# Performance work log

Measured on AMD Instinct MI355X. Metric: run time of the kernel, lower is better.

Reference implementation:

```python
import jax, jax.numpy as jnp
import numpy as np

G, NPG, K = 128, 1024, 16          # graphs, nodes per graph, kNN neighbors
NB_IN = 3
SLOPE = 0.01                        # torch.nn.LeakyReLU default negative_slope


def leaky(v):
    return jnp.where(v >= 0, v, SLOPE * v)


def knn_idx(pos, k):
    """pos: [G, n, 3] -> neighbor indices [G, n, k] within each graph, self excluded.
    Matches torch_geometric.nn.knn_graph (k nearest by Euclidean distance)."""
    sq = jnp.sum(pos * pos, axis=-1)                              # [G, n]
    d2 = sq[:, :, None] + sq[:, None, :] - 2.0 * jnp.einsum('gnd,gmd->gnm', pos, pos)
    n = pos.shape[1]
    d2 = d2 + jnp.eye(n, dtype=pos.dtype) * 1e9                   # exclude self-loops
    _, idx = jax.lax.top_k(-d2, k)                                # k smallest distances
    return idx


def edge_conv(h, idx, W1, b1, W2, b2):
    """EdgeConv with aggr='add': sum_j mlp(cat([x_i, x_j - x_i])).
    h: [G, n, F], idx: [G, n, k] -> [G, n, out]"""
    xj = jax.vmap(lambda hg, ig: hg[ig])(h, idx)                  # gather: [G, n, k, F]
    xi = jnp.broadcast_to(h[:, :, None, :], xj.shape)
    m = jnp.concatenate([xi, xj - xi], axis=-1)                   # [G, n, k, 2F]
    m = leaky(m @ W1 + b1)
    m = leaky(m @ W2 + b2)
    return jnp.sum(m, axis=2)                                     # scatter-add over k


def _linear_init(key, fin, fout):
    kw, kb = jax.random.split(key)
    lim = 1.0 / np.sqrt(fin)
    W = jax.random.uniform(kw, (fin, fout), jnp.float32, -lim, lim)
    b = jax.random.uniform(kb, (fout,), jnp.float32, -lim, lim)
    return W, b


def setup_inputs() -> dict:
    key = jax.random.key(0)
    ks = jax.random.split(key, 10)
    x = jax.random.normal(ks[0], (G * NPG, NB_IN), jnp.float32)
    batch = jnp.repeat(jnp.arange(G, dtype=jnp.int32), NPG)
    # layer 1 MLP: [2*3 -> 16 -> 16]; layer 2 MLP: [2*16 -> 16 -> 16]
    W1a, b1a = _linear_init(ks[1], 2 * NB_IN, 16)
    W2a, b2a = _linear_init(ks[2], 16, 16)
    W1b, b1b = _linear_init(ks[3], 2 * 16, 16)
    W2b, b2b = _linear_init(ks[4], 16, 16)
    # post-processing: [3+16+16=35 -> 16 -> 16]
    Wp1, bp1 = _linear_init(ks[5], 35, 16)
    Wp2, bp2 = _linear_init(ks[6], 16, 16)
    # readout: [16*3 poolings = 48 -> 128 -> 10]
    Wr1, br1 = _linear_init(ks[7], 48, 128)
    Wr2, br2 = _linear_init(ks[8], 128, 10)
    return {"x": x, "batch": batch,
            "W1a": W1a, "b1a": b1a, "W2a": W2a, "b2a": b2a,
            "W1b": W1b, "b1b": b1b, "W2b": W2b, "b2b": b2b,
            "Wp1": Wp1, "bp1": bp1, "Wp2": Wp2, "bp2": bp2,
            "Wr1": Wr1, "br1": br1, "Wr2": Wr2, "br2": br2}


def reference(x, batch, W1a, b1a, W2a, b2a, W1b, b1b, W2b, b2b,
              Wp1, bp1, Wp2, bp2, Wr1, br1, Wr2, br2):
    # equal-sized graphs sorted by batch id -> reshape to [G, n, F]
    h = x.reshape(G, NPG, -1)
    skips = [h]
    for (W1, b1, W2, b2) in ((W1a, b1a, W2a, b2a), (W1b, b1b, W2b, b2b)):
        idx = knn_idx(h[..., :3], K)       # features_subset = slice(0, 3)
        h = edge_conv(h, idx, W1, b1, W2, b2)
        skips.append(h)
    h = jnp.concatenate(skips, axis=-1)    # [G, n, 35]
    h = leaky(h @ Wp1 + bp1)
    h = leaky(h @ Wp2 + bp2)               # [G, n, 16]
    pooled = jnp.concatenate([h.min(axis=1), h.max(axis=1), h.mean(axis=1)], axis=-1)  # [G, 48]
    out = leaky(pooled @ Wr1 + br1) @ Wr2 + br2                   # [G, 10]
    return out
```

## Files before the change

### kernel.cpp

```cpp
#include <hip/hip_runtime.h>

#define NG 128
#define NN 1024
#define KK 16
#define HALF 512
#define PCAP 8
#define PMAX 16
#define SLOPE 0.01f
#define FINF 3.0e38f

typedef unsigned short u16;

__device__ __forceinline__ float leaky(float v) {
    return v >= 0.0f ? v : SLOPE * v;
}

__device__ __forceinline__ void sorted_insert(float (&bd)[KK], int (&bi)[KK],
                                              float d, int j) {
    bool c[KK];
#pragma unroll
    for (int t = 0; t < KK; ++t) c[t] = d < bd[t];
#pragma unroll
    for (int t = KK - 1; t >= 1; --t) {
        bd[t] = c[t] ? (c[t - 1] ? bd[t - 1] : d) : bd[t];
        bi[t] = c[t] ? (c[t - 1] ? bi[t - 1] : j) : bi[t];
    }
    bd[0] = c[0] ? d : bd[0];
    bi[0] = c[0] ? j : bi[0];
}

__device__ __forceinline__ void knn_scan_half(const float4* __restrict__ posq,
                                              float* __restrict__ pend_d,
                                              u16* __restrict__ pend_j,
                                              int tid, int i, int jlo,
                                              float (&bd)[KK], int (&bi)[KK]) {
    const float4 meq = posq[i];
    const float mex = -2.0f * meq.x, mey = -2.0f * meq.y, mez = -2.0f * meq.z;
    const float mew = meq.w;
#pragma unroll
    for (int t = 0; t < KK; ++t) { bd[t] = FINF; bi[t] = 0; }
    float T = FINF;
    int cnt = 0;

    for (int j0 = jlo; j0 < jlo + HALF; j0 += 8) {
        float4 p[8];
#pragma unroll
        for (int u = 0; u < 8; ++u) p[u] = posq[j0 + u];
#pragma unroll
        for (int u = 0; u < 8; ++u) {
            const int j = j0 + u;
            float d2 = fmaf(mex, p[u].x, fmaf(mey, p[u].y,
                          fmaf(mez, p[u].z, mew + p[u].w)));
            bool pass = (d2 < T) && (j != i);
            if (pass) {
                pend_d[tid + 256 * cnt] = d2;
                pend_j[tid + 256 * cnt] = (u16)j;
                ++cnt;
            }
        }
        if (__any(cnt >= PCAP)) {
#pragma unroll 1
            for (int s = 0; s < PMAX - 1; ++s) {
                float d = (s < cnt) ? pend_d[tid + 256 * s] : FINF;
                int j = pend_j[tid + 256 * s];
                if (__any(d < bd[KK - 1])) sorted_insert(bd, bi, d, j);
            }
            cnt = 0;
            T = bd[KK - 1];
        }
    }
#pragma unroll 1
    for (int s = 0; s < PCAP; ++s) {
        float d = (s < cnt) ? pend_d[tid + 256 * s] : FINF;
        int j = pend_j[tid + 256 * s];
        if (__any(d < bd[KK - 1])) sorted_insert(bd, bi, d, j);
    }
}

__device__ __forceinline__ void knn_body(const float4* __restrict__ posq,
                                         float* __restrict__ buf_d,
                                         u16* __restrict__ buf_j,
                                         int g, int chunk, int tid,
                                         u16* __restrict__ idx) {
    const int q = tid & 127;
    const int half = tid >> 7;
    const int i = chunk * 128 + q;

    float bd[KK];
    int bi[KK];
    knn_scan_half(posq, buf_d, buf_j, tid, i, half * HALF, bd, bi);

#pragma unroll
    for (int t = 0; t < KK; ++t) {
        buf_d[tid + 256 * t] = bd[t];
        buf_j[tid + 256 * t] = (u16)bi[t];
    }
    __syncthreads();

    if (tid < 128) {
        int ia = 0, ib = 0;
        unsigned int pack[8];
#pragma unroll
        for (int k = 0; k < KK; ++k) {
            float da = buf_d[tid + 256 * ia];
            float db = buf_d[(tid + 128) + 256 * ib];
            bool ta = da <= db;
            unsigned int j = ta ? (unsigned int)buf_j[tid + 256 * ia]
                               : (unsigned int)buf_j[(tid + 128) + 256 * ib];
            ia += ta ? 1 : 0;
            ib += ta ? 0 : 1;
            if ((k & 1) == 0) pack[k >> 1] = j;
            else pack[k >> 1] |= j << 16;
        }
        uint4* o4 = (uint4*)(idx + ((size_t)g * NN + i) * KK);
        o4[0] = make_uint4(pack[0], pack[1], pack[2], pack[3]);
        o4[1] = make_uint4(pack[4], pack[5], pack[6], pack[7]);
    }
}

__global__ __launch_bounds__(256) void knn1(
    const float* __restrict__ x, u16* __restrict__ idx)
{
    __shared__ float4 posq[NN];
    __shared__ float buf_d[256 * PMAX];
    __shared__ u16 buf_j[256 * PMAX];

    const int g = blockIdx.x >> 3;
    const int chunk = blockIdx.x & 7;
    const int tid = threadIdx.x;

    for (int n = tid; n < NN; n += 256) {
        const float* xp = x + (size_t)(g * NN + n) * 3;
        float px = xp[0], py = xp[1], pz = xp[2];
        posq[n] = make_float4(px, py, pz, px * px + py * py + pz * pz);
    }
    __syncthreads();

    knn_body(posq, buf_d, buf_j, g, chunk, tid, idx);
}

__global__ __launch_bounds__(256) void knn2(
    const float* __restrict__ h1, u16* __restrict__ idx)
{
    __shared__ float4 posq[NN];
    __shared__ float buf_d[256 * PMAX];
    __shared__ u16 buf_j[256 * PMAX];

    const int g = blockIdx.x >> 3;
    const int chunk = blockIdx.x & 7;
    const int tid = threadIdx.x;

    for (int n = tid; n < NN; n += 256) {
        const float4 a = *(const float4*)(h1 + (size_t)(g * NN + n) * 16);
        posq[n] = make_float4(a.x, a.y, a.z, a.x * a.x + a.y * a.y + a.z * a.z);
    }
    __syncthreads();

    knn_body(posq, buf_d, buf_j, g, chunk, tid, idx);
}

__device__ __forceinline__ void edge_pass(
    const float* __restrict__ u_lds,
    const float (&s1)[16],
    const u16* __restrict__ my_idx,
    const float* __restrict__ W2,
    const float* __restrict__ b2,
    float* __restrict__ out_row)
{
#pragma unroll 1
    for (int half = 0; half < 2; ++half) {
        float4 w2h[16][2];
#pragma unroll
        for (int f = 0; f < 16; ++f) {
            w2h[f][0] = *(const float4*)(W2 + f * 16 + half * 8);
            w2h[f][1] = *(const float4*)(W2 + f * 16 + half * 8 + 4);
        }
        float bb[8];
#pragma unroll
        for (int oo = 0; oo < 8; ++oo) bb[oo] = b2[half * 8 + oo];

        float acc[8];
#pragma unroll
        for (int oo = 0; oo < 8; ++oo) acc[oo] = 0.0f;

#pragma unroll 1
        for (int t = 0; t < KK; ++t) {
            const int j = my_idx[t];
            const float4* uj4 = (const float4*)(u_lds + j * 16);
            float4 u0 = uj4[0], u1 = uj4[1], u2 = uj4[2], u3 = uj4[3];
            float m1[16];
            m1[0]  = leaky(s1[0]  + u0.x);  m1[1]  = leaky(s1[1]  + u0.y);
            m1[2]  = leaky(s1[2]  + u0.z);  m1[3]  = leaky(s1[3]  + u0.w);
            m1[4]  = leaky(s1[4]  + u1.x);  m1[5]  = leaky(s1[5]  + u1.y);
            m1[6]  = leaky(s1[6]  + u1.z);  m1[7]  = leaky(s1[7]  + u1.w);
            m1[8]  = leaky(s1[8]  + u2.x);  m1[9]  = leaky(s1[9]  + u2.y);
            m1[10] = leaky(s1[10] + u2.z);  m1[11] = leaky(s1[11] + u2.w);
            m1[12] = leaky(s1[12] + u3.x);  m1[13] = leaky(s1[13] + u3.y);
            m1[14] = leaky(s1[14] + u3.z);  m1[15] = leaky(s1[15] + u3.w);

            float v[8];
#pragma unroll
            for (int oo = 0; oo < 8; ++oo) v[oo] = bb[oo];
#pragma unroll
            for (int f = 0; f < 16; ++f) {
                float4 wa = w2h[f][0], wb = w2h[f][1];
                v[0] += m1[f] * wa.x;  v[1] += m1[f] * wa.y;
                v[2] += m1[f] * wa.z;  v[3] += m1[f] * wa.w;
                v[4] += m1[f] * wb.x;  v[5] += m1[f] * wb.y;
                v[6] += m1[f] * wb.z;  v[7] += m1[f] * wb.w;
            }
#pragma unroll
            for (int oo = 0; oo < 8; ++oo) acc[oo] += leaky(v[oo]);
        }
        float4* o4 = (float4*)(out_row + half * 8);
        o4[0] = make_float4(acc[0], acc[1], acc[2], acc[3]);
        o4[1] = make_float4(acc[4], acc[5], acc[6], acc[7]);
    }
}

__global__ __launch_bounds__(256) void conv1(
    const float* __restrict__ x,
    const u16* __restrict__ idx,
    const float* __restrict__ W1,
    const float* __restrict__ b1,
    const float* __restrict__ W2,
    const float* __restrict__ b2,
    float* __restrict__ h1)
{
    __shared__ float u_lds[NN * 16];

    const int g = blockIdx.x >> 2;
    const int chunk = blockIdx.x & 3;
    const int tid = threadIdx.x;

    float wlo[3][16], whi[3][16];
#pragma unroll
    for (int c = 0; c < 3; ++c) {
#pragma unroll
        for (int q = 0; q < 4; ++q) {
            *(float4*)&wlo[c][q * 4] = *(const float4*)(W1 + c * 16 + q * 4);
            *(float4*)&whi[c][q * 4] = *(const float4*)(W1 + (3 + c) * 16 + q * 4);
        }
    }

#pragma unroll 1
    for (int r = 0; r < 4; ++r) {
        const int n = r * 256 + tid;
        const float* xp = x + ((size_t)g * NN + n) * 3;
        float px = xp[0], py = xp[1], pz = xp[2];
        float4* un = (float4*)(u_lds + n * 16);
#pragma unroll
        for (int q = 0; q < 4; ++q) {
            float4 uv;
            uv.x = px * whi[0][q * 4 + 0] + py * whi[1][q * 4 + 0] + pz * whi[2][q * 4 + 0];
            uv.y = px * whi[0][q * 4 + 1] + py * whi[1][q * 4 + 1] + pz * whi[2][q * 4 + 1];
            uv.z = px * whi[0][q * 4 + 2] + py * whi[1][q * 4 + 2] + pz * whi[2][q * 4 + 2];
            uv.w = px * whi[0][q * 4 + 3] + py * whi[1][q * 4 + 3] + pz * whi[2][q * 4 + 3];
            un[q] = uv;
        }
    }

    const int i = chunk * 256 + tid;
    const float* mp = x + ((size_t)g * NN + i) * 3;
    const float mxx = mp[0], myy = mp[1], mzz = mp[2];
    float s1[16];
#pragma unroll
    for (int o = 0; o < 16; ++o) {
        s1[o] = b1[o] + mxx * (wlo[0][o] - whi[0][o])
                      + myy * (wlo[1][o] - whi[1][o])
                      + mzz * (wlo[2][o] - whi[2][o]);
    }
    __syncthreads();

    edge_pass(u_lds, s1, idx + (size_t)(g * NN + i) * KK, W2, b2,
              h1 + (size_t)(g * NN + i) * 16);
}

__global__ __launch_bounds__(256) void conv2(
    const float* __restrict__ h1,
    const u16* __restrict__ idx,
    const float* __restrict__ W1,
    const float* __restrict__ b1,
    const float* __restrict__ W2,
    const float* __restrict__ b2,
    float* __restrict__ h2)
{
    __shared__ float tile[NN * 16];
    __shared__ float w1s[32 * 16];
    __shared__ float b1s[16];

    const int g = blockIdx.x >> 2;
    const int chunk = blockIdx.x & 3;
    const int tid = threadIdx.x;

    w1s[tid] = W1[tid];
    w1s[256 + tid] = W1[256 + tid];
    if (tid < 16) b1s[tid] = b1[tid];

    float4* t4 = (float4*)tile;
    const float4* src4 = (const float4*)(h1 + (size_t)g * NN * 16);
    for (int t = tid; t < NN * 4; t += 256) t4[t] = src4[t];
    __syncthreads();

    float s1[16];
#pragma unroll 1
    for (int r = 0; r < 4; ++r) {
        asm volatile("" ::: "memory");
        const int n = r * 256 + tid;
        float4 x0 = t4[n * 4 + 0], x1 = t4[n * 4 + 1];
        float4 x2 = t4[n * 4 + 2], x3 = t4[n * 4 + 3];
        float xr[16] = {x0.x, x0.y, x0.z, x0.w, x1.x, x1.y, x1.z, x1.w,
                        x2.x, x2.y, x2.z, x2.w, x3.x, x3.y, x3.z, x3.w};
        float uo[16];
#pragma unroll
        for (int og = 0; og < 4; ++og) {
            float a0 = 0.f, a1 = 0.f, a2 = 0.f, a3 = 0.f;
#pragma unroll
            for (int f = 0; f < 16; ++f) {
                float4 wv = *(const float4*)(w1s + (16 + f) * 16 + og * 4);
                a0 += xr[f] * wv.x; a1 += xr[f] * wv.y;
                a2 += xr[f] * wv.z; a3 += xr[f] * wv.w;
            }
            uo[og * 4 + 0] = a0; uo[og * 4 + 1] = a1;
            uo[og * 4 + 2] = a2; uo[og * 4 + 3] = a3;
        }
        if (r == chunk) {
            float t1[16];
#pragma unroll
            for (int og = 0; og < 4; ++og) {
                float a0 = 0.f, a1 = 0.f, a2 = 0.f, a3 = 0.f;
#pragma unroll
                for (int f = 0; f < 16; ++f) {
                    float4 wv = *(const float4*)(w1s + f * 16 + og * 4);
                    a0 += xr[f] * wv.x; a1 += xr[f] * wv.y;
                    a2 += xr[f] * wv.z; a3 += xr[f] * wv.w;
                }
                t1[og * 4 + 0] = a0; t1[og * 4 + 1] = a1;
                t1[og * 4 + 2] = a2; t1[og * 4 + 3] = a3;
            }
#pragma unroll
            for (int o = 0; o < 16; ++o) s1[o] = b1s[o] + t1[o] - uo[o];
        }
        t4[n * 4 + 0] = make_float4(uo[0], uo[1], uo[2], uo[3]);
        t4[n * 4 + 1] = make_float4(uo[4], uo[5], uo[6], uo[7]);
        t4[n * 4 + 2] = make_float4(uo[8], uo[9], uo[10], uo[11]);
        t4[n * 4 + 3] = make_float4(uo[12], uo[13], uo[14], uo[15]);
    }
    __syncthreads();

    const int i = chunk * 256 + tid;
    edge_pass(tile, s1, idx + (size_t)(g * NN + i) * KK, W2, b2,
              h2 + (size_t)(g * NN + i) * 16);
}

__global__ __launch_bounds__(256) void post_pool(
    const float* __restrict__ x,
    const float* __restrict__ h1,
    const float* __restrict__ h2,
    const float* __restrict__ Wp1, const float* __restrict__ bp1,
    const float* __restrict__ Wp2, const float* __restrict__ bp2,
    float* __restrict__ partial)
{
    __shared__ float wp1[35 * 16];
    __shared__ float wp2[16 * 16];
    __shared__ float sbp1[16], sbp2[16];
    __shared__ float red[3][4][16];

    const int g = blockIdx.x >> 2;
    const int chunk = blockIdx.x & 3;
    const int tid = threadIdx.x;

    wp2[tid] = Wp2[tid];
    for (int t = tid; t < 560; t += 256) wp1[t] = Wp1[t];
    if (tid < 16) { sbp1[tid] = bp1[tid]; sbp2[tid] = bp2[tid]; }
    __syncthreads();

    const int i = chunk * 256 + tid;
    const float* xp = x + (size_t)(g * NN + i) * 3;
    const float x0 = xp[0], x1 = xp[1], x2 = xp[2];
    const float4* p1v = (const float4*)(h1 + (size_t)(g * NN + i) * 16);
    float4 a0 = p1v[0], a1 = p1v[1], a2 = p1v[2], a3 = p1v[3];
    const float4* p2v = (const float4*)(h2 + (size_t)(g * NN + i) * 16);
    float4 c0 = p2v[0], c1 = p2v[1], c2 = p2v[2], c3 = p2v[3];

    float p1[16];
#pragma unroll
    for (int o = 0; o < 16; ++o) {
        float v = sbp1[o];
        v += x0 * wp1[0 * 16 + o];
        v += x1 * wp1[1 * 16 + o];
        v += x2 * wp1[2 * 16 + o];
        v += a0.x * wp1[3 * 16 + o];   v += a0.y * wp1[4 * 16 + o];
        v += a0.z * wp1[5 * 16 + o];   v += a0.w * wp1[6 * 16 + o];
        v += a1.x * wp1[7 * 16 + o];   v += a1.y * wp1[8 * 16 + o];
        v += a1.z * wp1[9 * 16 + o];   v += a1.w * wp1[10 * 16 + o];
        v += a2.x * wp1[11 * 16 + o];  v += a2.y * wp1[12 * 16 + o];
        v += a2.z * wp1[13 * 16 + o];  v += a2.w * wp1[14 * 16 + o];
        v += a3.x * wp1[15 * 16 + o];  v += a3.y * wp1[16 * 16 + o];
        v += a3.z * wp1[17 * 16 + o];  v += a3.w * wp1[18 * 16 + o];
        v += c0.x * wp1[19 * 16 + o];  v += c0.y * wp1[20 * 16 + o];
        v += c0.z * wp1[21 * 16 + o];  v += c0.w * wp1[22 * 16 + o];
        v += c1.x * wp1[23 * 16 + o];  v += c1.y * wp1[24 * 16 + o];
        v += c1.z * wp1[25 * 16 + o];  v += c1.w * wp1[26 * 16 + o];
        v += c2.x * wp1[27 * 16 + o];  v += c2.y * wp1[28 * 16 + o];
        v += c2.z * wp1[29 * 16 + o];  v += c2.w * wp1[30 * 16 + o];
        v += c3.x * wp1[31 * 16 + o];  v += c3.y * wp1[32 * 16 + o];
        v += c3.z * wp1[33 * 16 + o];  v += c3.w * wp1[34 * 16 + o];
        p1[o] = leaky(v);
    }

    float mn[16], mx[16], sm[16];
#pragma unroll
    for (int o = 0; o < 16; ++o) {
        float v = sbp2[o];
#pragma unroll
        for (int f = 0; f < 16; ++f) v += p1[f] * wp2[f * 16 + o];
        float p2 = leaky(v);
        mn[o] = p2; mx[o] = p2; sm[o] = p2;
    }

#pragma unroll
    for (int off = 32; off >= 1; off >>= 1) {
#pragma unroll
        for (int o = 0; o < 16; ++o) {
            mn[o] = fminf(mn[o], __shfl_xor(mn[o], off));
            mx[o] = fmaxf(mx[o], __shfl_xor(mx[o], off));
            sm[o] += __shfl_xor(sm[o], off);
        }
    }
    const int wave = tid >> 6;
    const int lane = tid & 63;
    if (lane == 0) {
#pragma unroll
        for (int o = 0; o < 16; ++o) {
            red[0][wave][o] = mn[o];
            red[1][wave][o] = mx[o];
            red[2][wave][o] = sm[o];
        }
    }
    __syncthreads();

    if (tid < 48) {
        const int stat = tid >> 4, o = tid & 15;
        float v;
        if (stat == 0)
            v = fminf(fminf(red[0][0][o], red[0][1][o]), fminf(red[0][2][o], red[0][3][o]));
        else if (stat == 1)
            v = fmaxf(fmaxf(red[1][0][o], red[1][1][o]), fmaxf(red[1][2][o], red[1][3][o]));
        else
            v = red[2][0][o] + red[2][1][o] + red[2][2][o] + red[2][3][o];
        partial[blockIdx.x * 48 + tid] = v;
    }
}

__global__ __launch_bounds__(128) void finalize(
    const float* __restrict__ partial,
    const float* __restrict__ Wr1, const float* __restrict__ br1,
    const float* __restrict__ Wr2, const float* __restrict__ br2,
    float* __restrict__ out)
{
    __shared__ float pooled[48];
    __shared__ float hidden[128];

    const int g = blockIdx.x;
    const int tid = threadIdx.x;

    if (tid < 48) {
        const int stat = tid >> 4;
        float a = partial[(g * 4 + 0) * 48 + tid];
        float b = partial[(g * 4 + 1) * 48 + tid];
        float c = partial[(g * 4 + 2) * 48 + tid];
        float d = partial[(g * 4 + 3) * 48 + tid];
        float v;
        if (stat == 0)      v = fminf(fminf(a, b), fminf(c, d));
        else if (stat == 1) v = fmaxf(fmaxf(a, b), fmaxf(c, d));
        else                v = (a + b + c + d) * (1.0f / NN);
        pooled[tid] = v;
    }
    __syncthreads();

    {
        float v = br1[tid];
#pragma unroll
        for (int f = 0; f < 48; ++f) v += pooled[f] * Wr1[f * 128 + tid];
        hidden[tid] = leaky(v);
    }
    __syncthreads();

    if (tid < 10) {
        float v = br2[tid];
#pragma unroll
        for (int f = 0; f < 128; ++f) v += hidden[f] * Wr2[f * 10 + tid];
        out[g * 10 + tid] = v;
    }
}

extern "C" void kernel_launch(void* const* d_in, const int* in_sizes, int n_in,
                              void* d_out, int out_size, void* d_ws, size_t ws_size,
                              hipStream_t stream) {
    const float* x   = (const float*)d_in[0];
    const float* W1a = (const float*)d_in[2];
    const float* b1a = (const float*)d_in[3];
    const float* W2a = (const float*)d_in[4];
    const float* b2a = (const float*)d_in[5];
    const float* W1b = (const float*)d_in[6];
    const float* b1b = (const float*)d_in[7];
    const float* W2b = (const float*)d_in[8];
    const float* b2b = (const float*)d_in[9];
    const float* Wp1 = (const float*)d_in[10];
    const float* bp1 = (const float*)d_in[11];
    const float* Wp2 = (const float*)d_in[12];
    const float* bp2 = (const float*)d_in[13];
    const float* Wr1 = (const float*)d_in[14];
    const float* br1 = (const float*)d_in[15];
    const float* Wr2 = (const float*)d_in[16];
    const float* br2 = (const float*)d_in[17];
    float* out = (float*)d_out;

    float* h1 = (float*)d_ws;
    float* h2 = h1 + (size_t)NG * NN * 16;
    u16* idx = (u16*)(h2 + (size_t)NG * NN * 16);
    float* partial = (float*)(idx + (size_t)NG * NN * KK);

    knn1<<<NG * 8, 256, 0, stream>>>(x, idx);
    conv1<<<NG * 4, 256, 0, stream>>>(x, idx, W1a, b1a, W2a, b2a, h1);
    knn2<<<NG * 8, 256, 0, stream>>>(h1, idx);
    conv2<<<NG * 4, 256, 0, stream>>>(h1, idx, W1b, b1b, W2b, b2b, h2);
    post_pool<<<NG * 4, 256, 0, stream>>>(x, h1, h2, Wp1, bp1, Wp2, bp2, partial);
    finalize<<<NG, 128, 0, stream>>>(partial, Wr1, br1, Wr2, br2, out);
}
```

Before: 572.6 us.

## Replace pending-buffer kNN with two-pass med3 threshold selection

The kNN selection now runs in two passes. The first pass keeps a branchless, distance-only sorted top-16 in registers using fmed3 per candidate, then merges the two halves through LDS to find the 16th-smallest distance. The second pass rescans the candidates, collects those at or below that threshold with their indices, and a final sorted insert produces the ordered index list. This removes the divergent pending-buffer flushes and index tracking from the hot loop, at the cost of computing distances twice, about 16 med3 ops per candidate, and extra syncs.

```diff
diff --git a/kernel.cpp b/kernel.cpp
--- a/kernel.cpp
+++ b/kernel.cpp
@@ -4,8 +4,6 @@
 #define NN 1024
 #define KK 16
 #define HALF 512
-#define PCAP 8
-#define PMAX 16
 #define SLOPE 0.01f
 #define FINF 3.0e38f
 
@@ -29,89 +27,109 @@
     bi[0] = c[0] ? j : bi[0];
 }
 
-__device__ __forceinline__ void knn_scan_half(const float4* __restrict__ posq,
-                                              float* __restrict__ pend_d,
-                                              u16* __restrict__ pend_j,
-                                              int tid, int i, int jlo,
-                                              float (&bd)[KK], int (&bi)[KK]) {
-    const float4 meq = posq[i];
-    const float mex = -2.0f * meq.x, mey = -2.0f * meq.y, mez = -2.0f * meq.z;
-    const float mew = meq.w;
-#pragma unroll
-    for (int t = 0; t < KK; ++t) { bd[t] = FINF; bi[t] = 0; }
-    float T = FINF;
-    int cnt = 0;
-
-    for (int j0 = jlo; j0 < jlo + HALF; j0 += 8) {
-        float4 p[8];
-#pragma unroll
-        for (int u = 0; u < 8; ++u) p[u] = posq[j0 + u];
-#pragma unroll
-        for (int u = 0; u < 8; ++u) {
-            const int j = j0 + u;
-            float d2 = fmaf(mex, p[u].x, fmaf(mey, p[u].y,
-                          fmaf(mez, p[u].z, mew + p[u].w)));
-            bool pass = (d2 < T) && (j != i);
-            if (pass) {
-                pend_d[tid + 256 * cnt] = d2;
-                pend_j[tid + 256 * cnt] = (u16)j;
-                ++cnt;
-            }
-        }
-        if (__any(cnt >= PCAP)) {
-#pragma unroll 1
-            for (int s = 0; s < PMAX - 1; ++s) {
-                float d = (s < cnt) ? pend_d[tid + 256 * s] : FINF;
-                int j = pend_j[tid + 256 * s];
-                if (__any(d < bd[KK - 1])) sorted_insert(bd, bi, d, j);
-            }
-            cnt = 0;
-            T = bd[KK - 1];
-        }
-    }
-#pragma unroll 1
-    for (int s = 0; s < PCAP; ++s) {
-        float d = (s < cnt) ? pend_d[tid + 256 * s] : FINF;
-        int j = pend_j[tid + 256 * s];
-        if (__any(d < bd[KK - 1])) sorted_insert(bd, bi, d, j);
-    }
-}
-
 __device__ __forceinline__ void knn_body(const float4* __restrict__ posq,
-                                         float* __restrict__ buf_d,
-                                         u16* __restrict__ buf_j,
+                                         float* __restrict__ pub_d,
+                                         u16* __restrict__ pend_j,
                                          int g, int chunk, int tid,
                                          u16* __restrict__ idx) {
     const int q = tid & 127;
     const int half = tid >> 7;
     const int i = chunk * 128 + q;
+    const int jlo = half * HALF;
+
+    const float4 meq = posq[i];
+    const float mex = -2.0f * meq.x, mey = -2.0f * meq.y, mez = -2.0f * meq.z;
+    const float mew = meq.w;
 
     float bd[KK];
-    int bi[KK];
-    knn_scan_half(posq, buf_d, buf_j, tid, i, half * HALF, bd, bi);
-
-#pragma unroll
-    for (int t = 0; t < KK; ++t) {
-        buf_d[tid + 256 * t] = bd[t];
-        buf_j[tid + 256 * t] = (u16)bi[t];
-    }
-    __syncthreads();
-
-    if (tid < 128) {
+#pragma unroll
+    for (int t = 0; t < KK; ++t) bd[t] = FINF;
+
+    for (int j0 = jlo; j0 < jlo + HALF; j0 += 8) {
+        float4 p[8];
+#pragma unroll
+        for (int u = 0; u < 8; ++u) p[u] = posq[j0 + u];
+#pragma unroll
+        for (int u = 0; u < 8; ++u) {
+            const int j = j0 + u;
+            float d2 = fmaf(mex, p[u].x, fmaf(mey, p[u].y,
+                          fmaf(mez, p[u].z, mew + p[u].w)));
+            d2 = (j == i) ? FINF : d2;
+#pragma unroll
+            for (int t = KK - 1; t >= 1; --t)
+                bd[t] = __builtin_amdgcn_fmed3f(d2, bd[t - 1], bd[t]);
+            bd[0] = fminf(bd[0], d2);
+        }
+    }
+
+#pragma unroll
+    for (int t = 0; t < KK; ++t) pub_d[tid + 256 * t] = bd[t];
+    __syncthreads();
+
+    float d16;
+    {
+        const int pr = tid ^ 128;
         int ia = 0, ib = 0;
-        unsigned int pack[8];
+        float v = FINF;
 #pragma unroll
         for (int k = 0; k < KK; ++k) {
-            float da = buf_d[tid + 256 * ia];
-            float db = buf_d[(tid + 128) + 256 * ib];
+            float da = pub_d[tid + 256 * ia];
+            float db = pub_d[pr + 256 * ib];
             bool ta = da <= db;
-            unsigned int j = ta ? (unsigned int)buf_j[tid + 256 * ia]
-                               : (unsigned int)buf_j[(tid + 128) + 256 * ib];
+            v = ta ? da : db;
             ia += ta ? 1 : 0;
             ib += ta ? 0 : 1;
-            if ((k & 1) == 0) pack[k >> 1] = j;
-            else pack[k >> 1] |= j << 16;
-        }
+        }
+        d16 = v;
+    }
+    __syncthreads();
+
+    int cnt = 0;
+    for (int j0 = jlo; j0 < jlo + HALF; j0 += 8) {
+        float4 p[8];
+#pragma unroll
+        for (int u = 0; u < 8; ++u) p[u] = posq[j0 + u];
+#pragma unroll
+        for (int u = 0; u < 8; ++u) {
+            const int j = j0 + u;
+            float d2 = fmaf(mex, p[u].x, fmaf(mey, p[u].y,
+                          fmaf(mez, p[u].z, mew + p[u].w)));
+            d2 = (j == i) ? FINF : d2;
+            if (d2 <= d16 && cnt < KK) {
+                pub_d[tid + 256 * cnt] = d2;
+                pend_j[tid + 256 * cnt] = (u16)j;
+                ++cnt;
+            }
+        }
+    }
+    pend_j[tid + 256 * 16] = (u16)cnt;
+    __syncthreads();
+
+    if (tid < 128) {
+        float sd[KK];
+        int si[KK];
+#pragma unroll
+        for (int t = 0; t < KK; ++t) { sd[t] = FINF; si[t] = 0; }
+        const int c0 = pend_j[tid + 256 * 16];
+        const int c1 = pend_j[(tid + 128) + 256 * 16];
+#pragma unroll 1
+        for (int s = 0; s < KK; ++s) {
+            bool a = s < c0;
+            float d = a ? pub_d[tid + 256 * s] : FINF;
+            int j = pend_j[tid + 256 * s];
+            if (__any(d < sd[KK - 1])) sorted_insert(sd, si, d, j);
+        }
+#pragma unroll 1
+        for (int s = 0; s < KK; ++s) {
+            bool a = s < c1;
+            float d = a ? pub_d[(tid + 128) + 256 * s] : FINF;
+            int j = pend_j[(tid + 128) + 256 * s];
+            if (__any(d < sd[KK - 1])) sorted_insert(sd, si, d, j);
+        }
+        unsigned int pack[8];
+#pragma unroll
+        for (int t = 0; t < KK; t += 2)
+            pack[t >> 1] = (unsigned int)si[t] | ((unsigned int)si[t + 1] << 16);
         uint4* o4 = (uint4*)(idx + ((size_t)g * NN + i) * KK);
         o4[0] = make_uint4(pack[0], pack[1], pack[2], pack[3]);
         o4[1] = make_uint4(pack[4], pack[5], pack[6], pack[7]);
@@ -122,8 +140,8 @@
     const float* __restrict__ x, u16* __restrict__ idx)
 {
     __shared__ float4 posq[NN];
-    __shared__ float buf_d[256 * PMAX];
-    __shared__ u16 buf_j[256 * PMAX];
+    __shared__ float pub_d[256 * 16];
+    __shared__ u16 pend_j[256 * 17];
 
     const int g = blockIdx.x >> 3;
     const int chunk = blockIdx.x & 7;
@@ -136,15 +154,15 @@
     }
     __syncthreads();
 
-    knn_body(posq, buf_d, buf_j, g, chunk, tid, idx);
+    knn_body(posq, pub_d, pend_j, g, chunk, tid, idx);
 }
 
 __global__ __launch_bounds__(256) void knn2(
     const float* __restrict__ h1, u16* __restrict__ idx)
 {
     __shared__ float4 posq[NN];
-    __shared__ float buf_d[256 * PMAX];
-    __shared__ u16 buf_j[256 * PMAX];
+    __shared__ float pub_d[256 * 16];
+    __shared__ u16 pend_j[256 * 17];
 
     const int g = blockIdx.x >> 3;
     const int chunk = blockIdx.x & 7;
@@ -156,7 +174,7 @@
     }
     __syncthreads();
 
-    knn_body(posq, buf_d, buf_j, g, chunk, tid, idx);
+    knn_body(posq, pub_d, pend_j, g, chunk, tid, idx);
 }
 
 __device__ __forceinline__ void edge_pass(
```

New measurement: 571.1 us. Within noise of the previous version (-0.3%).
